# Kernel tuning notes

Hardware: AMD Instinct MI355X
Metric: run time of the kernel (lower is better)

Reference implementation:

```python
import jax, jax.numpy as jnp
import numpy as np

B, T, D_IN, H, O = 64, 2048, 64, 256, 32
INTER, CMD, MOTOR = 135, 89, 32  # AutoNCP(256,32): command=int(0.4*224)=89, inter=135, motor=32
LAYER_DIMS = [(H, INTER), (INTER, CMD), (CMD, MOTOR)]  # (layer_input_dim, layer_units)


def setup_inputs() -> dict:
    key = jax.random.key(0)
    ks = iter(jax.random.split(key, 48))

    def lin(out_d, in_d):
        return jax.random.normal(next(ks), (out_d, in_d), jnp.float32) / np.sqrt(in_d)

    inp = {"x": jax.random.normal(next(ks), (B, T, D_IN), jnp.float32)}
    inp["Wp"] = lin(H, D_IN)
    inp["bp"] = jnp.zeros((H,), jnp.float32)
    for l, (ind, u) in enumerate(LAYER_DIMS):
        c = ind + u  # concat of [layer input, layer hidden]
        for nm in ("ff1", "ff2", "ta", "tb"):
            inp[f"W{nm}_{l}"] = lin(u, c)
            inp[f"b{nm}_{l}"] = jnp.zeros((u,), jnp.float32)
        inp[f"mask_{l}"] = jax.random.uniform(next(ks), (u, c)) < 0.5
    inp["Wh1"] = lin(H, O)
    inp["bh1"] = jnp.zeros((H,), jnp.float32)
    inp["Wh2"] = lin(O, H)
    inp["bh2"] = jnp.zeros((O,), jnp.float32)
    return inp


def _cfc_cell(xin, h, p):
    # ncps CfCCell, mode='default', no backbone, elapsed time ts = 1.0
    Wff1, bff1, Wff2, bff2, Wta, bta, Wtb, btb, mask = p
    z = jnp.concatenate([xin, h], axis=-1)
    m = mask.astype(Wff1.dtype)
    ff1 = jnp.tanh(z @ (Wff1 * m).T + bff1)
    ff2 = jnp.tanh(z @ (Wff2 * m).T + bff2)
    t_interp = jax.nn.sigmoid((z @ Wta.T + bta) * 1.0 + (z @ Wtb.T + btb))
    return ff1 * (1.0 - t_interp) + t_interp * ff2


def reference(x, Wp, bp,
              Wff1_0, bff1_0, Wff2_0, bff2_0, Wta_0, bta_0, Wtb_0, btb_0, mask_0,
              Wff1_1, bff1_1, Wff2_1, bff2_1, Wta_1, bta_1, Wtb_1, btb_1, mask_1,
              Wff1_2, bff1_2, Wff2_2, bff2_2, Wta_2, bta_2, Wtb_2, btb_2, mask_2,
              Wh1, bh1, Wh2, bh2):
    layers = [
        (Wff1_0, bff1_0, Wff2_0, bff2_0, Wta_0, bta_0, Wtb_0, btb_0, mask_0),
        (Wff1_1, bff1_1, Wff2_1, bff2_1, Wta_1, bta_1, Wtb_1, btb_1, mask_1),
        (Wff1_2, bff1_2, Wff2_2, bff2_2, Wta_2, bta_2, Wtb_2, btb_2, mask_2),
    ]
    proj = x @ Wp.T + bp  # (B,T,H) input projection
    b = x.shape[0]
    h_init = tuple(jnp.zeros((b, u), x.dtype) for _, u in LAYER_DIMS)

    def step(h, xt):
        inp = xt
        new_h = []
        for l in range(3):  # inter -> command -> motor layers of the NCP wiring
            hn = _cfc_cell(inp, h[l], layers[l])
            new_h.append(hn)
            inp = hn
        return tuple(new_h), new_h[-1]

    _, outs = jax.lax.scan(step, h_init, jnp.swapaxes(proj, 0, 1))
    cfc_out = jnp.swapaxes(outs, 0, 1)  # (B,T,O) motor-neuron outputs
    hdn = jax.nn.gelu(cfc_out @ Wh1.T + bh1, approximate=False)
    return hdn @ Wh2.T + bh2  # (B,T,O)
```

## Files before the change

### kernel.cpp

```cpp
#include <hip/hip_runtime.h>
#include <cstdint>
#include <cstddef>

typedef _Float16 half_t;
typedef half_t half2_t __attribute__((ext_vector_type(2)));

static constexpr int TTs = 2048;
static constexpr int BBn = 64;
static constexpr int DINn = 64;
static constexpr int HPn  = 256;
static constexpr int U0c = 135, C0c = 391, R0c = 405;
static constexpr int U1c = 89,  C1c = 224, R1c = 267;
static constexpr int U2c = 32,  C2c = 121, R2c = 96;
static constexpr size_t BTn = (size_t)BBn * TTs;

__device__ __forceinline__ float tanh_f(float x) {
    return 1.f - __fdividef(2.f, __expf(2.f * x) + 1.f);
}
__device__ __forceinline__ float sigm_f(float x) {
    return __fdividef(1.f, 1.f + __expf(-x));
}
__device__ __forceinline__ float cfc_comb(float y0, float y1, float y2) {
    float f1 = tanh_f(y0), f2 = tanh_f(y1), ti = sigm_f(y2);
    return f1 + ti * (f2 - f1);
}
__device__ __forceinline__ float qsum(float v) {
    v += __builtin_bit_cast(float, __builtin_amdgcn_update_dpp(
             0, __builtin_bit_cast(int, v), 0xB1, 0xF, 0xF, true));
    v += __builtin_bit_cast(float, __builtin_amdgcn_update_dpp(
             0, __builtin_bit_cast(int, v), 0x4E, 0xF, 0xF, true));
    return v;
}
__device__ __forceinline__ half2_t h2(unsigned u) { return __builtin_bit_cast(half2_t, u); }

__device__ __forceinline__ int mask_mode(const unsigned char* mp) {
    const unsigned* wp = (const unsigned*)mp;
    bool all01 = true, allf = true;
    for (int k = 0; k < 64; ++k) {
        unsigned w = wp[k];
        all01 = all01 && (w == 0u || w == 1u);
        allf  = allf  && (w == 0u || w == 0x3F800000u);
    }
    if (all01) return 0;
    if (allf)  return 1;
    return 2;
}
__device__ __forceinline__ bool mget(const unsigned char* mp, int mode, int idx) {
    if (mode == 0) return ((const int*)mp)[idx] != 0;
    if (mode == 1) return ((const float*)mp)[idx] != 0.f;
    return mp[idx] != 0;
}

__global__ void k_stack(const float* __restrict__ Wff1, const float* __restrict__ bff1,
                        const float* __restrict__ Wff2, const float* __restrict__ bff2,
                        const float* __restrict__ Wta,  const float* __restrict__ bta,
                        const float* __restrict__ Wtb,  const float* __restrict__ btb,
                        const unsigned char* __restrict__ maskraw,
                        int u, int c, int split,
                        float* __restrict__ outA, float* __restrict__ outB,
                        float* __restrict__ bias_out)
{
    const int mode = mask_mode(maskraw);
    const int total = 3 * u * c + 3 * u;
    for (int idx = blockIdx.x * blockDim.x + threadIdx.x; idx < total;
         idx += gridDim.x * blockDim.x) {
        if (idx < 3 * u * c) {
            int m = idx / (u * c);
            int rem = idx - m * u * c;
            int r = rem / c;
            int k = rem - r * c;
            float v;
            if (m == 2) {
                v = Wta[r * c + k] + Wtb[r * c + k];
            } else {
                bool mk = mget(maskraw, mode, r * c + k);
                float w = (m == 0) ? Wff1[r * c + k] : Wff2[r * c + k];
                v = mk ? w : 0.f;
            }
            int R = m * u + r;
            if (k < split) outA[(size_t)R * split + k] = v;
            else           outB[(size_t)R * (c - split) + (k - split)] = v;
        } else {
            int j = idx - 3 * u * c;
            int m = j / u, r = j - m * u;
            bias_out[j] = (m == 0) ? bff1[r] : ((m == 1) ? bff2[r] : (bta[r] + btb[r]));
        }
    }
}

__global__ void k_comb(const float* __restrict__ Wx0s, const float* __restrict__ Wp,
                       float* __restrict__ Wcomb)
{
    const int r = blockIdx.x;
    const int d = threadIdx.x;
    float acc = 0.f;
    for (int k = 0; k < HPn; ++k) acc += Wx0s[(size_t)r * HPn + k] * Wp[(size_t)k * DINn + d];
    Wcomb[(size_t)r * DINn + d] = acc;
}

__global__ void k_biasc(const float* __restrict__ Wx0s, const float* __restrict__ bp,
                        const float* __restrict__ b0, float* __restrict__ b0c,
                        const float* __restrict__ Wh2, float* __restrict__ Wh2T)
{
    const int i = blockIdx.x * blockDim.x + threadIdx.x;
    if (i < R0c) {
        float a = b0[i];
        for (int k = 0; k < HPn; ++k) a += Wx0s[(size_t)i * HPn + k] * bp[k];
        b0c[i] = a;
    }
    if (i < HPn * 32) {
        int h = i >> 5, o = i & 31;
        Wh2T[i] = Wh2[(size_t)o * HPn + h];
    }
}

__global__ void k_pack(const float* __restrict__ Wcb, const float* __restrict__ Wh0s,
                       const float* __restrict__ W1s, const float* __restrict__ W2s,
                       half_t* __restrict__ W0h, half_t* __restrict__ W1h,
                       half_t* __restrict__ W2h)
{
    const int N0 = R0c * 224, N1 = R1c * 224, N2 = R2c * 128;
    for (int idx = blockIdx.x * blockDim.x + threadIdx.x; idx < N0 + N1 + N2;
         idx += gridDim.x * blockDim.x) {
        if (idx < N0) {
            int r = idx / 224, c = idx - r * 224;
            float v = (c < 64) ? Wcb[(size_t)r * 64 + c]
                               : ((c < 199) ? Wh0s[(size_t)r * 135 + (c - 64)] : 0.f);
            W0h[idx] = (half_t)v;
        } else if (idx < N0 + N1) {
            int i = idx - N0;
            W1h[i] = (half_t)W1s[i];
        } else {
            int i = idx - N0 - N1;
            int r = i / 128, c = i - r * 128;
            W2h[i] = (half_t)((c < 121) ? W2s[(size_t)r * 121 + c] : 0.f);
        }
    }
}

#define PIN4(v) asm volatile("" : "+v"((v).x), "+v"((v).y), "+v"((v).z), "+v"((v).w))
#define BAR() asm volatile("s_waitcnt lgkmcnt(0)\n\ts_barrier" ::: "memory")

#define LD7(a,b,c,d,e,f,g, ptr) { const uint4* _p = (const uint4*)(ptr); \
    a=_p[0]; b=_p[1]; c=_p[2]; d=_p[3]; e=_p[4]; f=_p[5]; g=_p[6]; }
#define LD4(a,b,c,d, ptr) { const uint4* _p = (const uint4*)(ptr); \
    a=_p[0]; b=_p[1]; c=_p[2]; d=_p[3]; }
#define Z7(a,b,c,d,e,f,g) a=z4u; b=z4u; c=z4u; d=z4u; e=z4u; f=z4u; g=z4u;
#define D4(acc, W, F) \
    acc = __builtin_amdgcn_fdot2(h2((W).x), __builtin_bit_cast(half2_t,(F).x), acc, false); \
    acc = __builtin_amdgcn_fdot2(h2((W).y), __builtin_bit_cast(half2_t,(F).y), acc, false); \
    acc = __builtin_amdgcn_fdot2(h2((W).z), __builtin_bit_cast(half2_t,(F).z), acc, false); \
    acc = __builtin_amdgcn_fdot2(h2((W).w), __builtin_bit_cast(half2_t,(F).w), acc, false);
#define DR7(acc, A,B,C,D,E,F,G) D4(acc,A,f0) D4(acc,B,f1) D4(acc,C,f2) \
    D4(acc,D,f3) D4(acc,E,f4) D4(acc,F,f5) D4(acc,G,f6)
#define DR4(acc, A,B,C,D) D4(acc,A,f0) D4(acc,B,f1) D4(acc,C,f2) D4(acc,D,f3)

__global__ __launch_bounds__(512) void k_scan(
    const half_t* __restrict__ W0h,
    const half_t* __restrict__ W1h,
    const half_t* __restrict__ W2h,
    const float* __restrict__ b0c,
    const float* __restrict__ b1s,
    const float* __restrict__ b2s,
    const float* __restrict__ x,
    float* __restrict__ cfc)
{
    const int t = threadIdx.x;
    const int b = blockIdx.x;
    const int q = t & 3;

    __shared__ float4 z0v[2][28];
    __shared__ float4 z1v[2][28];
    __shared__ float4 z2v[2][16];

    {
        float4* zz = (float4*)z0v;
        for (int i = t; i < 144; i += 512) zz[i] = make_float4(0.f, 0.f, 0.f, 0.f);
    }

    const bool gL0 = (t < 256);
    const bool gL1 = (t >= 256) && (t < 448);
    const int s0 = t >> 2;
    const int s1 = (t - 256) >> 2;
    const int s2 = (t - 448) >> 2;
    const int xi = t - 448;

    const uint4 z4u = make_uint4(0u, 0u, 0u, 0u);
    uint4 w00,w01,w02,w03,w04,w05,w06, w07,w08,w09,w10,w11,w12,w13;
    uint4 w14,w15,w16,w17,w18,w19,w20, w21,w22,w23,w24,w25,w26,w27;
    uint4 w28,w29,w30,w31,w32,w33,w34, w35,w36,w37,w38,w39,w40,w41;
    uint4 w42,w43,w44;
    Z7(w00,w01,w02,w03,w04,w05,w06) Z7(w07,w08,w09,w10,w11,w12,w13)
    Z7(w14,w15,w16,w17,w18,w19,w20) Z7(w21,w22,w23,w24,w25,w26,w27)
    Z7(w28,w29,w30,w31,w32,w33,w34) Z7(w35,w36,w37,w38,w39,w40,w41)
    w42 = z4u; w43 = z4u; w44 = z4u;

    float bA0=0.f,bA1=0.f,bA2=0.f, bB0=0.f,bB1=0.f,bB2=0.f, bX0=0.f,bX1=0.f,bX2=0.f;
    bool vB = false, vX = false;

    if (gL0) {
        const size_t cq = 56 * q;
        LD7(w00,w01,w02,w03,w04,w05,w06, W0h + (size_t)(s0      ) * 224 + cq)
        LD7(w07,w08,w09,w10,w11,w12,w13, W0h + (size_t)(s0 + 135) * 224 + cq)
        LD7(w14,w15,w16,w17,w18,w19,w20, W0h + (size_t)(s0 + 270) * 224 + cq)
        LD7(w21,w22,w23,w24,w25,w26,w27, W0h + (size_t)(s0 +  64) * 224 + cq)
        LD7(w28,w29,w30,w31,w32,w33,w34, W0h + (size_t)(s0 + 199) * 224 + cq)
        LD7(w35,w36,w37,w38,w39,w40,w41, W0h + (size_t)(s0 + 334) * 224 + cq)
        bA0 = b0c[s0];      bA1 = b0c[135 + s0]; bA2 = b0c[270 + s0];
        bB0 = b0c[64 + s0]; bB1 = b0c[199 + s0]; bB2 = b0c[334 + s0];
        vB = true;
    } else if (gL1) {
        const size_t cq = 56 * q;
        const bool vA = (s1 <= 44);
        vB = (s1 <= 43);
        const int ua = vA ? s1 : 0;
        const int ub = vB ? 45 + s1 : 0;
        LD7(w00,w01,w02,w03,w04,w05,w06, W1h + (size_t)(ua      ) * 224 + cq)
        LD7(w07,w08,w09,w10,w11,w12,w13, W1h + (size_t)(ua +  89) * 224 + cq)
        LD7(w14,w15,w16,w17,w18,w19,w20, W1h + (size_t)(ua + 178) * 224 + cq)
        LD7(w21,w22,w23,w24,w25,w26,w27, W1h + (size_t)(ub      ) * 224 + cq)
        LD7(w28,w29,w30,w31,w32,w33,w34, W1h + (size_t)(ub +  89) * 224 + cq)
        LD7(w35,w36,w37,w38,w39,w40,w41, W1h + (size_t)(ub + 178) * 224 + cq)
        if (!vA) { Z7(w00,w01,w02,w03,w04,w05,w06) Z7(w07,w08,w09,w10,w11,w12,w13)
                   Z7(w14,w15,w16,w17,w18,w19,w20) }
        if (!vB) { Z7(w21,w22,w23,w24,w25,w26,w27) Z7(w28,w29,w30,w31,w32,w33,w34)
                   Z7(w35,w36,w37,w38,w39,w40,w41) }
        if (vA) { bA0 = b1s[ua]; bA1 = b1s[89 + ua]; bA2 = b1s[178 + ua]; }
        if (vB) { bB0 = b1s[ub]; bB1 = b1s[89 + ub]; bB2 = b1s[178 + ub]; }
    } else {
        const size_t c2 = 32 * q;
        LD4(w00,w01,w02,w03, W2h + (size_t)(s2     ) * 128 + c2)
        LD4(w04,w05,w06,w07, W2h + (size_t)(s2 + 32) * 128 + c2)
        LD4(w08,w09,w10,w11, W2h + (size_t)(s2 + 64) * 128 + c2)
        LD4(w12,w13,w14,w15, W2h + (size_t)(s2 + 16) * 128 + c2)
        LD4(w16,w17,w18,w19, W2h + (size_t)(s2 + 48) * 128 + c2)
        LD4(w20,w21,w22,w23, W2h + (size_t)(s2 + 80) * 128 + c2)
        vX = (s2 < 7);
        const int ux = vX ? 128 + s2 : 128;
        const size_t cq = 56 * q;
        LD7(w24,w25,w26,w27,w28,w29,w30, W0h + (size_t)(ux      ) * 224 + cq)
        LD7(w31,w32,w33,w34,w35,w36,w37, W0h + (size_t)(ux + 135) * 224 + cq)
        LD7(w38,w39,w40,w41,w42,w43,w44, W0h + (size_t)(ux + 270) * 224 + cq)
        if (!vX) { Z7(w24,w25,w26,w27,w28,w29,w30) Z7(w31,w32,w33,w34,w35,w36,w37)
                   Z7(w38,w39,w40,w41,w42,w43,w44) }
        bA0 = b2s[s2];      bA1 = b2s[32 + s2]; bA2 = b2s[64 + s2];
        bB0 = b2s[16 + s2]; bB1 = b2s[48 + s2]; bB2 = b2s[80 + s2];
        if (vX) { bX0 = b0c[ux]; bX1 = b0c[135 + ux]; bX2 = b0c[270 + ux]; }
    }
    PIN4(w00);PIN4(w01);PIN4(w02);PIN4(w03);PIN4(w04);PIN4(w05);PIN4(w06);
    PIN4(w07);PIN4(w08);PIN4(w09);PIN4(w10);PIN4(w11);PIN4(w12);PIN4(w13);
    PIN4(w14);PIN4(w15);PIN4(w16);PIN4(w17);PIN4(w18);PIN4(w19);PIN4(w20);
    PIN4(w21);PIN4(w22);PIN4(w23);PIN4(w24);PIN4(w25);PIN4(w26);PIN4(w27);
    PIN4(w28);PIN4(w29);PIN4(w30);PIN4(w31);PIN4(w32);PIN4(w33);PIN4(w34);
    PIN4(w35);PIN4(w36);PIN4(w37);PIN4(w38);PIN4(w39);PIN4(w40);PIN4(w41);
    PIN4(w42);PIN4(w43);PIN4(w44);

    const float* xb = x + (size_t)b * TTs * DINn;
    float* cfb = cfc + (size_t)b * TTs * 32;

    __syncthreads();
    if (xi >= 0) ((half_t*)&z0v[0][0])[xi] = (half_t)xb[xi];
    __syncthreads();

#pragma unroll 1
    for (int k = 0; k < TTs + 2; ++k) {
        const int p = k & 1;
        half_t* z0n = (half_t*)&z0v[p ^ 1][0];
        half_t* z1n = (half_t*)&z1v[p ^ 1][0];
        half_t* z2n = (half_t*)&z2v[p ^ 1][0];

        if (gL0) {
            const float4* zc = &z0v[p][q * 7];
            float4 f0 = zc[0], f1 = zc[1], f2 = zc[2], f3 = zc[3],
                   f4 = zc[4], f5 = zc[5], f6 = zc[6];
            float a0=0.f,a1=0.f,a2=0.f,a3=0.f,a4=0.f,a5=0.f;
            DR7(a0, w00,w01,w02,w03,w04,w05,w06)
            DR7(a1, w07,w08,w09,w10,w11,w12,w13)
            DR7(a2, w14,w15,w16,w17,w18,w19,w20)
            DR7(a3, w21,w22,w23,w24,w25,w26,w27)
            DR7(a4, w28,w29,w30,w31,w32,w33,w34)
            DR7(a5, w35,w36,w37,w38,w39,w40,w41)
            a0=qsum(a0); a1=qsum(a1); a2=qsum(a2);
            a3=qsum(a3); a4=qsum(a4); a5=qsum(a5);
            if (q == 0) {
                float h1v = cfc_comb(a0 + bA0, a1 + bA1, a2 + bA2);
                half_t hh1 = (half_t)h1v;
                z0n[64 + s0]  = hh1;
                z1n[s0]       = hh1;
                float h2v = cfc_comb(a3 + bB0, a4 + bB1, a5 + bB2);
                half_t hh2 = (half_t)h2v;
                z0n[128 + s0] = hh2;
                z1n[64 + s0]  = hh2;
            }
        } else if (gL1) {
            const float4* zc = &z1v[p][q * 7];
            float4 f0 = zc[0], f1 = zc[1], f2 = zc[2], f3 = zc[3],
                   f4 = zc[4], f5 = zc[5], f6 = zc[6];
            float a0=0.f,a1=0.f,a2=0.f,a3=0.f,a4=0.f,a5=0.f;
            DR7(a0, w00,w01,w02,w03,w04,w05,w06)
            DR7(a1, w07,w08,w09,w10,w11,w12,w13)
            DR7(a2, w14,w15,w16,w17,w18,w19,w20)
            DR7(a3, w21,w22,w23,w24,w25,w26,w27)
            DR7(a4, w28,w29,w30,w31,w32,w33,w34)
            DR7(a5, w35,w36,w37,w38,w39,w40,w41)
            a0=qsum(a0); a1=qsum(a1); a2=qsum(a2);
            a3=qsum(a3); a4=qsum(a4); a5=qsum(a5);
            if (q == 0 && k >= 1) {
                if (s1 <= 44) {
                    float hv = cfc_comb(a0 + bA0, a1 + bA1, a2 + bA2);
                    half_t hh = (half_t)hv;
                    z1n[135 + s1] = hh;
                    z2n[s1]       = hh;
                }
                if (vB) {
                    float hv = cfc_comb(a3 + bB0, a4 + bB1, a5 + bB2);
                    half_t hh = (half_t)hv;
                    z1n[180 + s1] = hh;
                    z2n[45 + s1]  = hh;
                }
            }
        } else {
            int tn = k + 1; if (tn > TTs - 1) tn = TTs - 1;
            float xnext = xb[(size_t)tn * DINn + xi];
            {
                const float4* zc = &z2v[p][q * 4];
                float4 f0 = zc[0], f1 = zc[1], f2 = zc[2], f3 = zc[3];
                float a0=0.f,a1=0.f,a2=0.f,a3=0.f,a4=0.f,a5=0.f;
                DR4(a0, w00,w01,w02,w03)
                DR4(a1, w04,w05,w06,w07)
                DR4(a2, w08,w09,w10,w11)
                DR4(a3, w12,w13,w14,w15)
                DR4(a4, w16,w17,w18,w19)
                DR4(a5, w20,w21,w22,w23)
                a0=qsum(a0); a1=qsum(a1); a2=qsum(a2);
                a3=qsum(a3); a4=qsum(a4); a5=qsum(a5);
                if (q == 0 && k >= 2) {
                    float hv0 = cfc_comb(a0 + bA0, a1 + bA1, a2 + bA2);
                    z2n[89 + s2]  = (half_t)hv0;
                    cfb[(size_t)(k - 2) * 32 + s2] = hv0;
                    float hv1 = cfc_comb(a3 + bB0, a4 + bB1, a5 + bB2);
                    z2n[105 + s2] = (half_t)hv1;
                    cfb[(size_t)(k - 2) * 32 + 16 + s2] = hv1;
                }
            }
            if (vX) {
                const float4* zc = &z0v[p][q * 7];
                float4 f0 = zc[0], f1 = zc[1], f2 = zc[2], f3 = zc[3],
                       f4 = zc[4], f5 = zc[5], f6 = zc[6];
                float c0=0.f,c1=0.f,c2=0.f;
                DR7(c0, w24,w25,w26,w27,w28,w29,w30)
                DR7(c1, w31,w32,w33,w34,w35,w36,w37)
                DR7(c2, w38,w39,w40,w41,w42,w43,w44)
                c0=qsum(c0); c1=qsum(c1); c2=qsum(c2);
                if (q == 0) {
                    float hv = cfc_comb(c0 + bX0, c1 + bX1, c2 + bX2);
                    half_t hh = (half_t)hv;
                    z0n[192 + s2] = hh;
                    z1n[128 + s2] = hh;
                }
            }
            z0n[xi] = (half_t)xnext;
        }
        BAR();
    }
}

__global__ __launch_bounds__(256) void k_head(float* io,
                                              const float* __restrict__ Wh1,
                                              const float* __restrict__ bh1,
                                              const float* __restrict__ Wh2T,
                                              const float* __restrict__ bh2)
{
    const int bt = blockIdx.x * 256 + threadIdx.x;
    float c32[32];
    const float4* cp = (const float4*)(io + (size_t)bt * 32);
#pragma unroll
    for (int k = 0; k < 8; ++k) {
        float4 v = cp[k];
        c32[4 * k] = v.x; c32[4 * k + 1] = v.y; c32[4 * k + 2] = v.z; c32[4 * k + 3] = v.w;
    }
    float acc[32];
#pragma unroll
    for (int o = 0; o < 32; ++o) acc[o] = bh2[o];
#pragma unroll 1
    for (int h = 0; h < HPn; ++h) {
        float ss = bh1[h];
        const float* w1r = Wh1 + (size_t)h * 32;
#pragma unroll
        for (int k = 0; k < 32; ++k) ss += c32[k] * w1r[k];
        float g = 0.5f * ss * (1.f + erff(ss * 0.70710678118654752440f));
        const float* w2r = Wh2T + (size_t)h * 32;
#pragma unroll
        for (int o = 0; o < 32; ++o) acc[o] += g * w2r[o];
    }
    float4* op = (float4*)(io + (size_t)bt * 32);
#pragma unroll
    for (int k = 0; k < 8; ++k) {
        float4 v;
        v.x = acc[4 * k]; v.y = acc[4 * k + 1]; v.z = acc[4 * k + 2]; v.w = acc[4 * k + 3];
        op[k] = v;
    }
}

extern "C" void kernel_launch(void* const* d_in, const int* in_sizes, int n_in,
                              void* d_out, int out_size, void* d_ws, size_t ws_size,
                              hipStream_t stream)
{
    (void)in_sizes; (void)n_in; (void)out_size; (void)ws_size;
    const float* x      = (const float*)d_in[0];
    const float* Wp     = (const float*)d_in[1];
    const float* bp     = (const float*)d_in[2];
    const float* Wff1_0 = (const float*)d_in[3];
    const float* bff1_0 = (const float*)d_in[4];
    const float* Wff2_0 = (const float*)d_in[5];
    const float* bff2_0 = (const float*)d_in[6];
    const float* Wta_0  = (const float*)d_in[7];
    const float* bta_0  = (const float*)d_in[8];
    const float* Wtb_0  = (const float*)d_in[9];
    const float* btb_0  = (const float*)d_in[10];
    const unsigned char* mask_0 = (const unsigned char*)d_in[11];
    const float* Wff1_1 = (const float*)d_in[12];
    const float* bff1_1 = (const float*)d_in[13];
    const float* Wff2_1 = (const float*)d_in[14];
    const float* bff2_1 = (const float*)d_in[15];
    const float* Wta_1  = (const float*)d_in[16];
    const float* bta_1  = (const float*)d_in[17];
    const float* Wtb_1  = (const float*)d_in[18];
    const float* btb_1  = (const float*)d_in[19];
    const unsigned char* mask_1 = (const unsigned char*)d_in[20];
    const float* Wff1_2 = (const float*)d_in[21];
    const float* bff1_2 = (const float*)d_in[22];
    const float* Wff2_2 = (const float*)d_in[23];
    const float* bff2_2 = (const float*)d_in[24];
    const float* Wta_2  = (const float*)d_in[25];
    const float* bta_2  = (const float*)d_in[26];
    const float* Wtb_2  = (const float*)d_in[27];
    const float* btb_2  = (const float*)d_in[28];
    const unsigned char* mask_2 = (const unsigned char*)d_in[29];
    const float* Wh1    = (const float*)d_in[30];
    const float* bh1    = (const float*)d_in[31];
    const float* Wh2    = (const float*)d_in[32];
    const float* bh2    = (const float*)d_in[33];

    float* ws = (float*)d_ws;
    size_t o = 0;
    float* Wh0s = ws + o; o += (size_t)R0c * U0c;
    float* Wx0s = ws + o; o += (size_t)R0c * HPn;
    float* b0s  = ws + o; o += R0c; o += 3;
    float* Wcb  = ws + o; o += (size_t)R0c * DINn;
    float* b0c  = ws + o; o += R0c; o += 3;
    float* W1s  = ws + o; o += (size_t)R1c * C1c;
    float* b1s  = ws + o; o += R1c; o += 1;
    float* W2s  = ws + o; o += (size_t)R2c * C2c;
    float* b2s  = ws + o; o += R2c;
    float* Wh2T = ws + o; o += (size_t)HPn * 32;
    half_t* W0h = (half_t*)(ws + o); o += (size_t)R0c * 224 / 2;
    half_t* W1h = (half_t*)(ws + o); o += (size_t)R1c * 224 / 2;
    half_t* W2h = (half_t*)(ws + o); o += (size_t)R2c * 128 / 2;

    k_stack<<<128, 256, 0, stream>>>(Wff1_0, bff1_0, Wff2_0, bff2_0, Wta_0, bta_0, Wtb_0, btb_0,
                                     mask_0, U0c, C0c, HPn, Wx0s, Wh0s, b0s);
    k_stack<<<64, 256, 0, stream>>>(Wff1_1, bff1_1, Wff2_1, bff2_1, Wta_1, bta_1, Wtb_1, btb_1,
                                    mask_1, U1c, C1c, C1c, W1s, W1s, b1s);
    k_stack<<<16, 256, 0, stream>>>(Wff1_2, bff1_2, Wff2_2, bff2_2, Wta_2, bta_2, Wtb_2, btb_2,
                                    mask_2, U2c, C2c, C2c, W2s, W2s, b2s);
    k_comb<<<R0c, DINn, 0, stream>>>(Wx0s, Wp, Wcb);
    k_biasc<<<32, 256, 0, stream>>>(Wx0s, bp, b0s, b0c, Wh2, Wh2T);
    k_pack<<<320, 256, 0, stream>>>(Wcb, Wh0s, W1s, W2s, W0h, W1h, W2h);
    k_scan<<<BBn, 512, 0, stream>>>(W0h, W1h, W2h, b0c, b1s, b2s, x, (float*)d_out);
    k_head<<<(int)(BTn / 256), 256, 0, stream>>>((float*)d_out, Wh1, bh1, Wh2T, bh2);
}
```

Before: 3.249 ms.

## Keep recurrent weights in AGPRs and move layer-0 tail weights to LDS

The per-thread weight fragments for the recurrent scan move from VGPRs into accumulation registers (AGPRs), written once at setup with v_accvgpr_write and read back with v_accvgpr_read before each dot product. The extra layer-0 tail weights used by the last wave group now live in a shared-memory table instead of registers. The aim is to cut VGPR pressure and spilling in the 512-thread scan kernel. The cost is extra accvgpr read instructions and LDS loads inside the serial time loop.

```diff
diff --git a/kernel.cpp b/kernel.cpp
--- a/kernel.cpp
+++ b/kernel.cpp
@@ -138,22 +138,44 @@
     }
 }
 
-#define PIN4(v) asm volatile("" : "+v"((v).x), "+v"((v).y), "+v"((v).z), "+v"((v).w))
 #define BAR() asm volatile("s_waitcnt lgkmcnt(0)\n\ts_barrier" ::: "memory")
 
-#define LD7(a,b,c,d,e,f,g, ptr) { const uint4* _p = (const uint4*)(ptr); \
-    a=_p[0]; b=_p[1]; c=_p[2]; d=_p[3]; e=_p[4]; f=_p[5]; g=_p[6]; }
-#define LD4(a,b,c,d, ptr) { const uint4* _p = (const uint4*)(ptr); \
-    a=_p[0]; b=_p[1]; c=_p[2]; d=_p[3]; }
-#define Z7(a,b,c,d,e,f,g) a=z4u; b=z4u; c=z4u; d=z4u; e=z4u; f=z4u; g=z4u;
+struct ag4 { unsigned x, y, z, w; };
+#define AW(dst, s) asm volatile( \
+    "v_accvgpr_write_b32 %0, %4\n\t" \
+    "v_accvgpr_write_b32 %1, %5\n\t" \
+    "v_accvgpr_write_b32 %2, %6\n\t" \
+    "v_accvgpr_write_b32 %3, %7" \
+    : "=a"((dst).x), "=a"((dst).y), "=a"((dst).z), "=a"((dst).w) \
+    : "v"((s).x), "v"((s).y), "v"((s).z), "v"((s).w));
+#define AR(d, s) asm volatile( \
+    "v_accvgpr_read_b32 %0, %4\n\t" \
+    "v_accvgpr_read_b32 %1, %5\n\t" \
+    "v_accvgpr_read_b32 %2, %6\n\t" \
+    "v_accvgpr_read_b32 %3, %7" \
+    : "=v"((d).x), "=v"((d).y), "=v"((d).z), "=v"((d).w) \
+    : "a"((s).x), "a"((s).y), "a"((s).z), "a"((s).w));
+
 #define D4(acc, W, F) \
     acc = __builtin_amdgcn_fdot2(h2((W).x), __builtin_bit_cast(half2_t,(F).x), acc, false); \
     acc = __builtin_amdgcn_fdot2(h2((W).y), __builtin_bit_cast(half2_t,(F).y), acc, false); \
     acc = __builtin_amdgcn_fdot2(h2((W).z), __builtin_bit_cast(half2_t,(F).z), acc, false); \
     acc = __builtin_amdgcn_fdot2(h2((W).w), __builtin_bit_cast(half2_t,(F).w), acc, false);
-#define DR7(acc, A,B,C,D,E,F,G) D4(acc,A,f0) D4(acc,B,f1) D4(acc,C,f2) \
-    D4(acc,D,f3) D4(acc,E,f4) D4(acc,F,f5) D4(acc,G,f6)
-#define DR4(acc, A,B,C,D) D4(acc,A,f0) D4(acc,B,f1) D4(acc,C,f2) D4(acc,D,f3)
+#define DA4(acc, agw, F) { uint4 _t; AR(_t, agw) D4(acc, _t, F) }
+#define DR7A(acc, A,B,C,D,E,F,G) DA4(acc,A,f0) DA4(acc,B,f1) DA4(acc,C,f2) \
+    DA4(acc,D,f3) DA4(acc,E,f4) DA4(acc,F,f5) DA4(acc,G,f6)
+#define DR4A(acc, A,B,C,D) DA4(acc,A,f0) DA4(acc,B,f1) DA4(acc,C,f2) DA4(acc,D,f3)
+#define AW7(w0,w1,w2,w3,w4,w5,w6, ptr, kill) { \
+    const uint4* _p = (const uint4*)(ptr); \
+    uint4 t0=_p[0],t1=_p[1],t2=_p[2],t3=_p[3],t4=_p[4],t5=_p[5],t6=_p[6]; \
+    if (kill) { t0=z4u;t1=z4u;t2=z4u;t3=z4u;t4=z4u;t5=z4u;t6=z4u; } \
+    AW(w0,t0) AW(w1,t1) AW(w2,t2) AW(w3,t3) AW(w4,t4) AW(w5,t5) AW(w6,t6) \
+    __builtin_amdgcn_sched_barrier(0); }
+#define AW4B(w0,w1,w2,w3, ptr) { \
+    const uint4* _p = (const uint4*)(ptr); \
+    uint4 t0=_p[0],t1=_p[1],t2=_p[2],t3=_p[3]; \
+    AW(w0,t0) AW(w1,t1) AW(w2,t2) AW(w3,t3) \
+    __builtin_amdgcn_sched_barrier(0); }
 
 __global__ __launch_bounds__(512) void k_scan(
     const half_t* __restrict__ W0h,
@@ -172,6 +194,7 @@
     __shared__ float4 z0v[2][28];
     __shared__ float4 z1v[2][28];
     __shared__ float4 z2v[2][16];
+    __shared__ uint4  lwv[28][21];
 
     {
         float4* zz = (float4*)z0v;
@@ -186,26 +209,21 @@
     const int xi = t - 448;
 
     const uint4 z4u = make_uint4(0u, 0u, 0u, 0u);
-    uint4 w00,w01,w02,w03,w04,w05,w06, w07,w08,w09,w10,w11,w12,w13;
-    uint4 w14,w15,w16,w17,w18,w19,w20, w21,w22,w23,w24,w25,w26,w27;
-    uint4 w28,w29,w30,w31,w32,w33,w34, w35,w36,w37,w38,w39,w40,w41;
-    uint4 w42,w43,w44;
-    Z7(w00,w01,w02,w03,w04,w05,w06) Z7(w07,w08,w09,w10,w11,w12,w13)
-    Z7(w14,w15,w16,w17,w18,w19,w20) Z7(w21,w22,w23,w24,w25,w26,w27)
-    Z7(w28,w29,w30,w31,w32,w33,w34) Z7(w35,w36,w37,w38,w39,w40,w41)
-    w42 = z4u; w43 = z4u; w44 = z4u;
+    ag4 w00,w01,w02,w03,w04,w05,w06, w07,w08,w09,w10,w11,w12,w13;
+    ag4 w14,w15,w16,w17,w18,w19,w20, w21,w22,w23,w24,w25,w26,w27;
+    ag4 w28,w29,w30,w31,w32,w33,w34, w35,w36,w37,w38,w39,w40,w41;
 
     float bA0=0.f,bA1=0.f,bA2=0.f, bB0=0.f,bB1=0.f,bB2=0.f, bX0=0.f,bX1=0.f,bX2=0.f;
     bool vB = false, vX = false;
 
     if (gL0) {
         const size_t cq = 56 * q;
-        LD7(w00,w01,w02,w03,w04,w05,w06, W0h + (size_t)(s0      ) * 224 + cq)
-        LD7(w07,w08,w09,w10,w11,w12,w13, W0h + (size_t)(s0 + 135) * 224 + cq)
-        LD7(w14,w15,w16,w17,w18,w19,w20, W0h + (size_t)(s0 + 270) * 224 + cq)
-        LD7(w21,w22,w23,w24,w25,w26,w27, W0h + (size_t)(s0 +  64) * 224 + cq)
-        LD7(w28,w29,w30,w31,w32,w33,w34, W0h + (size_t)(s0 + 199) * 224 + cq)
-        LD7(w35,w36,w37,w38,w39,w40,w41, W0h + (size_t)(s0 + 334) * 224 + cq)
+        AW7(w00,w01,w02,w03,w04,w05,w06, W0h + (size_t)(s0      ) * 224 + cq, false)
+        AW7(w07,w08,w09,w10,w11,w12,w13, W0h + (size_t)(s0 + 135) * 224 + cq, false)
+        AW7(w14,w15,w16,w17,w18,w19,w20, W0h + (size_t)(s0 + 270) * 224 + cq, false)
+        AW7(w21,w22,w23,w24,w25,w26,w27, W0h + (size_t)(s0 +  64) * 224 + cq, false)
+        AW7(w28,w29,w30,w31,w32,w33,w34, W0h + (size_t)(s0 + 199) * 224 + cq, false)
+        AW7(w35,w36,w37,w38,w39,w40,w41, W0h + (size_t)(s0 + 334) * 224 + cq, false)
         bA0 = b0c[s0];      bA1 = b0c[135 + s0]; bA2 = b0c[270 + s0];
         bB0 = b0c[64 + s0]; bB1 = b0c[199 + s0]; bB2 = b0c[334 + s0];
         vB = true;
@@ -215,45 +233,39 @@
         vB = (s1 <= 43);
         const int ua = vA ? s1 : 0;
         const int ub = vB ? 45 + s1 : 0;
-        LD7(w00,w01,w02,w03,w04,w05,w06, W1h + (size_t)(ua      ) * 224 + cq)
-        LD7(w07,w08,w09,w10,w11,w12,w13, W1h + (size_t)(ua +  89) * 224 + cq)
-        LD7(w14,w15,w16,w17,w18,w19,w20, W1h + (size_t)(ua + 178) * 224 + cq)
-        LD7(w21,w22,w23,w24,w25,w26,w27, W1h + (size_t)(ub      ) * 224 + cq)
-        LD7(w28,w29,w30,w31,w32,w33,w34, W1h + (size_t)(ub +  89) * 224 + cq)
-        LD7(w35,w36,w37,w38,w39,w40,w41, W1h + (size_t)(ub + 178) * 224 + cq)
-        if (!vA) { Z7(w00,w01,w02,w03,w04,w05,w06) Z7(w07,w08,w09,w10,w11,w12,w13)
-                   Z7(w14,w15,w16,w17,w18,w19,w20) }
-        if (!vB) { Z7(w21,w22,w23,w24,w25,w26,w27) Z7(w28,w29,w30,w31,w32,w33,w34)
-                   Z7(w35,w36,w37,w38,w39,w40,w41) }
+        AW7(w00,w01,w02,w03,w04,w05,w06, W1h + (size_t)(ua      ) * 224 + cq, !vA)
+        AW7(w07,w08,w09,w10,w11,w12,w13, W1h + (size_t)(ua +  89) * 224 + cq, !vA)
+        AW7(w14,w15,w16,w17,w18,w19,w20, W1h + (size_t)(ua + 178) * 224 + cq, !vA)
+        AW7(w21,w22,w23,w24,w25,w26,w27, W1h + (size_t)(ub      ) * 224 + cq, !vB)
+        AW7(w28,w29,w30,w31,w32,w33,w34, W1h + (size_t)(ub +  89) * 224 + cq, !vB)
+        AW7(w35,w36,w37,w38,w39,w40,w41, W1h + (size_t)(ub + 178) * 224 + cq, !vB)
         if (vA) { bA0 = b1s[ua]; bA1 = b1s[89 + ua]; bA2 = b1s[178 + ua]; }
         if (vB) { bB0 = b1s[ub]; bB1 = b1s[89 + ub]; bB2 = b1s[178 + ub]; }
     } else {
         const size_t c2 = 32 * q;
-        LD4(w00,w01,w02,w03, W2h + (size_t)(s2     ) * 128 + c2)
-        LD4(w04,w05,w06,w07, W2h + (size_t)(s2 + 32) * 128 + c2)
-        LD4(w08,w09,w10,w11, W2h + (size_t)(s2 + 64) * 128 + c2)
-        LD4(w12,w13,w14,w15, W2h + (size_t)(s2 + 16) * 128 + c2)
-        LD4(w16,w17,w18,w19, W2h + (size_t)(s2 + 48) * 128 + c2)
-        LD4(w20,w21,w22,w23, W2h + (size_t)(s2 + 80) * 128 + c2)
+        AW4B(w00,w01,w02,w03, W2h + (size_t)(s2     ) * 128 + c2)
+        AW4B(w04,w05,w06,w07, W2h + (size_t)(s2 + 32) * 128 + c2)
+        AW4B(w08,w09,w10,w11, W2h + (size_t)(s2 + 64) * 128 + c2)
+        AW4B(w12,w13,w14,w15, W2h + (size_t)(s2 + 16) * 128 + c2)
+        AW4B(w16,w17,w18,w19, W2h + (size_t)(s2 + 48) * 128 + c2)
+        AW4B(w20,w21,w22,w23, W2h + (size_t)(s2 + 80) * 128 + c2)
         vX = (s2 < 7);
-        const int ux = vX ? 128 + s2 : 128;
-        const size_t cq = 56 * q;
-        LD7(w24,w25,w26,w27,w28,w29,w30, W0h + (size_t)(ux      ) * 224 + cq)
-        LD7(w31,w32,w33,w34,w35,w36,w37, W0h + (size_t)(ux + 135) * 224 + cq)
-        LD7(w38,w39,w40,w41,w42,w43,w44, W0h + (size_t)(ux + 270) * 224 + cq)
-        if (!vX) { Z7(w24,w25,w26,w27,w28,w29,w30) Z7(w31,w32,w33,w34,w35,w36,w37)
-                   Z7(w38,w39,w40,w41,w42,w43,w44) }
+        if (vX) {
+            const int ux = 128 + s2;
+            const size_t cq = 56 * q;
+            uint4* dst = &lwv[s2 * 4 + q][0];
+            const uint4* p0 = (const uint4*)(W0h + (size_t)(ux      ) * 224 + cq);
+            const uint4* p1 = (const uint4*)(W0h + (size_t)(ux + 135) * 224 + cq);
+            const uint4* p2 = (const uint4*)(W0h + (size_t)(ux + 270) * 224 + cq);
+#pragma unroll
+            for (int j = 0; j < 7; ++j) { dst[j] = p0[j]; dst[7 + j] = p1[j]; dst[14 + j] = p2[j]; }
+            bX0 = b0c[ux]; bX1 = b0c[135 + ux]; bX2 = b0c[270 + ux];
+        }
         bA0 = b2s[s2];      bA1 = b2s[32 + s2]; bA2 = b2s[64 + s2];
         bB0 = b2s[16 + s2]; bB1 = b2s[48 + s2]; bB2 = b2s[80 + s2];
-        if (vX) { bX0 = b0c[ux]; bX1 = b0c[135 + ux]; bX2 = b0c[270 + ux]; }
-    }
-    PIN4(w00);PIN4(w01);PIN4(w02);PIN4(w03);PIN4(w04);PIN4(w05);PIN4(w06);
-    PIN4(w07);PIN4(w08);PIN4(w09);PIN4(w10);PIN4(w11);PIN4(w12);PIN4(w13);
-    PIN4(w14);PIN4(w15);PIN4(w16);PIN4(w17);PIN4(w18);PIN4(w19);PIN4(w20);
-    PIN4(w21);PIN4(w22);PIN4(w23);PIN4(w24);PIN4(w25);PIN4(w26);PIN4(w27);
-    PIN4(w28);PIN4(w29);PIN4(w30);PIN4(w31);PIN4(w32);PIN4(w33);PIN4(w34);
-    PIN4(w35);PIN4(w36);PIN4(w37);PIN4(w38);PIN4(w39);PIN4(w40);PIN4(w41);
-    PIN4(w42);PIN4(w43);PIN4(w44);
+    }
+    asm volatile("" : "+v"(bA0),"+v"(bA1),"+v"(bA2),"+v"(bB0),"+v"(bB1),"+v"(bB2),
+                      "+v"(bX0),"+v"(bX1),"+v"(bX2));
 
     const float* xb = x + (size_t)b * TTs * DINn;
     float* cfb = cfc + (size_t)b * TTs * 32;
@@ -274,12 +286,12 @@
             float4 f0 = zc[0], f1 = zc[1], f2 = zc[2], f3 = zc[3],
                    f4 = zc[4], f5 = zc[5], f6 = zc[6];
             float a0=0.f,a1=0.f,a2=0.f,a3=0.f,a4=0.f,a5=0.f;
-            DR7(a0, w00,w01,w02,w03,w04,w05,w06)
-            DR7(a1, w07,w08,w09,w10,w11,w12,w13)
-            DR7(a2, w14,w15,w16,w17,w18,w19,w20)
-            DR7(a3, w21,w22,w23,w24,w25,w26,w27)
-            DR7(a4, w28,w29,w30,w31,w32,w33,w34)
-            DR7(a5, w35,w36,w37,w38,w39,w40,w41)
+            DR7A(a0, w00,w01,w02,w03,w04,w05,w06)
+            DR7A(a1, w07,w08,w09,w10,w11,w12,w13)
+            DR7A(a2, w14,w15,w16,w17,w18,w19,w20)
+            DR7A(a3, w21,w22,w23,w24,w25,w26,w27)
+            DR7A(a4, w28,w29,w30,w31,w32,w33,w34)
+            DR7A(a5, w35,w36,w37,w38,w39,w40,w41)
             a0=qsum(a0); a1=qsum(a1); a2=qsum(a2);
             a3=qsum(a3); a4=qsum(a4); a5=qsum(a5);
             if (q == 0) {
@@ -297,12 +309,12 @@
             float4 f0 = zc[0], f1 = zc[1], f2 = zc[2], f3 = zc[3],
                    f4 = zc[4], f5 = zc[5], f6 = zc[6];
             float a0=0.f,a1=0.f,a2=0.f,a3=0.f,a4=0.f,a5=0.f;
-            DR7(a0, w00,w01,w02,w03,w04,w05,w06)
-            DR7(a1, w07,w08,w09,w10,w11,w12,w13)
-            DR7(a2, w14,w15,w16,w17,w18,w19,w20)
-            DR7(a3, w21,w22,w23,w24,w25,w26,w27)
-            DR7(a4, w28,w29,w30,w31,w32,w33,w34)
-            DR7(a5, w35,w36,w37,w38,w39,w40,w41)
+            DR7A(a0, w00,w01,w02,w03,w04,w05,w06)
+            DR7A(a1, w07,w08,w09,w10,w11,w12,w13)
+            DR7A(a2, w14,w15,w16,w17,w18,w19,w20)
+            DR7A(a3, w21,w22,w23,w24,w25,w26,w27)
+            DR7A(a4, w28,w29,w30,w31,w32,w33,w34)
+            DR7A(a5, w35,w36,w37,w38,w39,w40,w41)
             a0=qsum(a0); a1=qsum(a1); a2=qsum(a2);
             a3=qsum(a3); a4=qsum(a4); a5=qsum(a5);
             if (q == 0 && k >= 1) {
@@ -326,12 +338,12 @@
                 const float4* zc = &z2v[p][q * 4];
                 float4 f0 = zc[0], f1 = zc[1], f2 = zc[2], f3 = zc[3];
                 float a0=0.f,a1=0.f,a2=0.f,a3=0.f,a4=0.f,a5=0.f;
-                DR4(a0, w00,w01,w02,w03)
-                DR4(a1, w04,w05,w06,w07)
-                DR4(a2, w08,w09,w10,w11)
-                DR4(a3, w12,w13,w14,w15)
-                DR4(a4, w16,w17,w18,w19)
-                DR4(a5, w20,w21,w22,w23)
+                DR4A(a0, w00,w01,w02,w03)
+                DR4A(a1, w04,w05,w06,w07)
+                DR4A(a2, w08,w09,w10,w11)
+                DR4A(a3, w12,w13,w14,w15)
+                DR4A(a4, w16,w17,w18,w19)
+                DR4A(a5, w20,w21,w22,w23)
                 a0=qsum(a0); a1=qsum(a1); a2=qsum(a2);
                 a3=qsum(a3); a4=qsum(a4); a5=qsum(a5);
                 if (q == 0 && k >= 2) {
@@ -347,10 +359,20 @@
                 const float4* zc = &z0v[p][q * 7];
                 float4 f0 = zc[0], f1 = zc[1], f2 = zc[2], f3 = zc[3],
                        f4 = zc[4], f5 = zc[5], f6 = zc[6];
+                const uint4* lwp = &lwv[s2 * 4 + q][0];
                 float c0=0.f,c1=0.f,c2=0.f;
-                DR7(c0, w24,w25,w26,w27,w28,w29,w30)
-                DR7(c1, w31,w32,w33,w34,w35,w36,w37)
-                DR7(c2, w38,w39,w40,w41,w42,w43,w44)
+                { uint4 _t=lwp[0];  D4(c0,_t,f0) } { uint4 _t=lwp[1];  D4(c0,_t,f1) }
+                { uint4 _t=lwp[2];  D4(c0,_t,f2) } { uint4 _t=lwp[3];  D4(c0,_t,f3) }
+                { uint4 _t=lwp[4];  D4(c0,_t,f4) } { uint4 _t=lwp[5];  D4(c0,_t,f5) }
+                { uint4 _t=lwp[6];  D4(c0,_t,f6) }
+                { uint4 _t=lwp[7];  D4(c1,_t,f0) } { uint4 _t=lwp[8];  D4(c1,_t,f1) }
+                { uint4 _t=lwp[9];  D4(c1,_t,f2) } { uint4 _t=lwp[10]; D4(c1,_t,f3) }
+                { uint4 _t=lwp[11]; D4(c1,_t,f4) } { uint4 _t=lwp[12]; D4(c1,_t,f5) }
+                { uint4 _t=lwp[13]; D4(c1,_t,f6) }
+                { uint4 _t=lwp[14]; D4(c2,_t,f0) } { uint4 _t=lwp[15]; D4(c2,_t,f1) }
+                { uint4 _t=lwp[16]; D4(c2,_t,f2) } { uint4 _t=lwp[17]; D4(c2,_t,f3) }
+                { uint4 _t=lwp[18]; D4(c2,_t,f4) } { uint4 _t=lwp[19]; D4(c2,_t,f5) }
+                { uint4 _t=lwp[20]; D4(c2,_t,f6) }
                 c0=qsum(c0); c1=qsum(c1); c2=qsum(c2);
                 if (q == 0) {
                     float hv = cfc_comb(c0 + bX0, c1 + bX1, c2 + bX2);
```

Measured after the change: 4.660 ms. 1.43x slower.

## Pre-convert input to fp16 and prefetch next timestep's input one iteration ahead

Applied to the files above, without the earlier changes.

Adds a pre-pass kernel that converts x to half precision in workspace when space allows. The scan kernel then reads half values and loads the input for step k+2 during step k, keeping it in a register so global load latency is hidden behind a full iteration instead of being exposed before the barrier. It also removes the empty inline asm that pinned weight registers, leaving register allocation to the compiler, which could raise spilling or register pressure.

```diff
diff --git a/kernel.cpp b/kernel.cpp
--- a/kernel.cpp
+++ b/kernel.cpp
@@ -138,7 +138,16 @@
     }
 }
 
-#define PIN4(v) asm volatile("" : "+v"((v).x), "+v"((v).y), "+v"((v).z), "+v"((v).w))
+__global__ __launch_bounds__(256) void k_xh(const float* __restrict__ x,
+                                            half_t* __restrict__ xh)
+{
+    size_t i = ((size_t)blockIdx.x * 256 + threadIdx.x) * 4;
+    if (i >= BTn * (size_t)DINn) return;
+    float4 v = *(const float4*)(x + i);
+    half_t* o = xh + i;
+    o[0] = (half_t)v.x; o[1] = (half_t)v.y; o[2] = (half_t)v.z; o[3] = (half_t)v.w;
+}
+
 #define BAR() asm volatile("s_waitcnt lgkmcnt(0)\n\ts_barrier" ::: "memory")
 
 #define LD7(a,b,c,d,e,f,g, ptr) { const uint4* _p = (const uint4*)(ptr); \
@@ -163,6 +172,8 @@
     const float* __restrict__ b1s,
     const float* __restrict__ b2s,
     const float* __restrict__ x,
+    const half_t* __restrict__ xh,
+    int use_xh,
     float* __restrict__ cfc)
 {
     const int t = threadIdx.x;
@@ -247,19 +258,17 @@
         bB0 = b2s[16 + s2]; bB1 = b2s[48 + s2]; bB2 = b2s[80 + s2];
         if (vX) { bX0 = b0c[ux]; bX1 = b0c[135 + ux]; bX2 = b0c[270 + ux]; }
     }
-    PIN4(w00);PIN4(w01);PIN4(w02);PIN4(w03);PIN4(w04);PIN4(w05);PIN4(w06);
-    PIN4(w07);PIN4(w08);PIN4(w09);PIN4(w10);PIN4(w11);PIN4(w12);PIN4(w13);
-    PIN4(w14);PIN4(w15);PIN4(w16);PIN4(w17);PIN4(w18);PIN4(w19);PIN4(w20);
-    PIN4(w21);PIN4(w22);PIN4(w23);PIN4(w24);PIN4(w25);PIN4(w26);PIN4(w27);
-    PIN4(w28);PIN4(w29);PIN4(w30);PIN4(w31);PIN4(w32);PIN4(w33);PIN4(w34);
-    PIN4(w35);PIN4(w36);PIN4(w37);PIN4(w38);PIN4(w39);PIN4(w40);PIN4(w41);
-    PIN4(w42);PIN4(w43);PIN4(w44);
-
-    const float* xb = x + (size_t)b * TTs * DINn;
+
+    const float*  xb  = x  + (size_t)b * TTs * DINn;
+    const half_t* xbh = xh + (size_t)b * TTs * DINn;
     float* cfb = cfc + (size_t)b * TTs * 32;
 
     __syncthreads();
-    if (xi >= 0) ((half_t*)&z0v[0][0])[xi] = (half_t)xb[xi];
+    half_t xr = (half_t)0.f;
+    if (xi >= 0) {
+        ((half_t*)&z0v[0][0])[xi] = use_xh ? xbh[xi] : (half_t)xb[xi];
+        xr = use_xh ? xbh[DINn + xi] : (half_t)xb[DINn + xi];
+    }
     __syncthreads();
 
 #pragma unroll 1
@@ -320,8 +329,6 @@
                 }
             }
         } else {
-            int tn = k + 1; if (tn > TTs - 1) tn = TTs - 1;
-            float xnext = xb[(size_t)tn * DINn + xi];
             {
                 const float4* zc = &z2v[p][q * 4];
                 float4 f0 = zc[0], f1 = zc[1], f2 = zc[2], f3 = zc[3];
@@ -359,7 +366,10 @@
                     z1n[128 + s2] = hh;
                 }
             }
-            z0n[xi] = (half_t)xnext;
+            z0n[xi] = xr;
+            int tn = k + 2; if (tn > TTs - 1) tn = TTs - 1;
+            xr = use_xh ? xbh[(size_t)tn * DINn + xi]
+                        : (half_t)xb[(size_t)tn * DINn + xi];
         }
         BAR();
     }
@@ -406,7 +416,7 @@
                               void* d_out, int out_size, void* d_ws, size_t ws_size,
                               hipStream_t stream)
 {
-    (void)in_sizes; (void)n_in; (void)out_size; (void)ws_size;
+    (void)in_sizes; (void)n_in; (void)out_size;
     const float* x      = (const float*)d_in[0];
     const float* Wp     = (const float*)d_in[1];
     const float* bp     = (const float*)d_in[2];
@@ -457,6 +467,9 @@
     half_t* W0h = (half_t*)(ws + o); o += (size_t)R0c * 224 / 2;
     half_t* W1h = (half_t*)(ws + o); o += (size_t)R1c * 224 / 2;
     half_t* W2h = (half_t*)(ws + o); o += (size_t)R2c * 128 / 2;
+    half_t* xhp = (half_t*)(ws + o);
+    const size_t xh_floats = BTn * (size_t)DINn / 2;
+    const int use_xh = (ws_size >= (o + xh_floats) * sizeof(float)) ? 1 : 0;
 
     k_stack<<<128, 256, 0, stream>>>(Wff1_0, bff1_0, Wff2_0, bff2_0, Wta_0, bta_0, Wtb_0, btb_0,
                                      mask_0, U0c, C0c, HPn, Wx0s, Wh0s, b0s);
@@ -467,6 +480,10 @@
     k_comb<<<R0c, DINn, 0, stream>>>(Wx0s, Wp, Wcb);
     k_biasc<<<32, 256, 0, stream>>>(Wx0s, bp, b0s, b0c, Wh2, Wh2T);
     k_pack<<<320, 256, 0, stream>>>(Wcb, Wh0s, W1s, W2s, W0h, W1h, W2h);
-    k_scan<<<BBn, 512, 0, stream>>>(W0h, W1h, W2h, b0c, b1s, b2s, x, (float*)d_out);
+    if (use_xh) {
+        k_xh<<<(int)(BTn * DINn / 4 / 256), 256, 0, stream>>>(x, xhp);
+    }
+    k_scan<<<BBn, 512, 0, stream>>>(W0h, W1h, W2h, b0c, b1s, b2s, x, xhp, use_xh,
+                                    (float*)d_out);
     k_head<<<(int)(BTn / 256), 256, 0, stream>>>((float*)d_out, Wh1, bh1, Wh2T, bh2);
 }
```

Measured after the change: 3.336 ms. 1.03x slower.
